# Kernel optimization log

Hardware: AMD Instinct MI355X
Metric: run time of the kernel (lower is better)

The kernel has to match this reference:

```python
import jax, jax.numpy as jnp
import numpy as np

B, N, F_IN = 4, 8000, 3          # batch, electrons per event, (x,y,z) features
HID, S, T = 128, 1024, 1024      # MLP hidden, n_sensors, waveform_ticks
INV_SQRT_2PI = 0.3989422804


def _mlp(x, W1, b1, W2, b2):
    h = jax.nn.relu(x @ W1 + b1)
    return h @ W2 + b2


def setup_inputs() -> dict:
    key = jax.random.key(0)
    ks = jax.random.split(key, 12)
    simulator_input = jax.random.normal(ks[0], (B, N, F_IN), dtype=jnp.float32)
    # z positions in tick units, spread across the waveform
    z_positions = jax.random.uniform(ks[1], (B, N), dtype=jnp.float32) * (T - 1)
    mask = jnp.ones((B, N, 1), dtype=jnp.float32)
    s1 = 1.0 / np.sqrt(F_IN)
    s2 = 1.0 / np.sqrt(HID)
    Wp1 = jax.random.normal(ks[2], (F_IN, HID), dtype=jnp.float32) * s1
    bp1 = jnp.zeros((HID,), dtype=jnp.float32)
    Wp2 = jax.random.normal(ks[3], (HID, S), dtype=jnp.float32) * s2
    bp2 = jnp.zeros((S,), dtype=jnp.float32)
    Wa1 = jax.random.normal(ks[4], (F_IN, HID), dtype=jnp.float32) * s1
    ba1 = jnp.zeros((HID,), dtype=jnp.float32)
    Wa2 = jax.random.normal(ks[5], (HID, S), dtype=jnp.float32) * s2
    ba2 = jnp.zeros((S,), dtype=jnp.float32)
    nn_bin_sigma = 5.0 * jnp.ones((1,), dtype=jnp.float32)  # self.variable init
    return dict(simulator_input=simulator_input, z_positions=z_positions, mask=mask,
                Wp1=Wp1, bp1=bp1, Wp2=Wp2, bp2=bp2,
                Wa1=Wa1, ba1=ba1, Wa2=Wa2, ba2=ba2,
                nn_bin_sigma=nn_bin_sigma)


def reference(simulator_input, z_positions, mask,
              Wp1, bp1, Wp2, bp2, Wa1, ba1, Wa2, ba2, nn_bin_sigma):
    # sensor response per electron: sigmoid(prob MLP) * amp MLP * mask  -> [B,N,S]
    sensor_probs = jax.nn.sigmoid(_mlp(simulator_input, Wp1, bp1, Wp2, bp2))
    el_light_amp = _mlp(simulator_input, Wa1, ba1, Wa2, ba2)
    response_of_sensors = el_light_amp * sensor_probs * mask

    # Gaussian binning kernel over waveform ticks: [B,N,T]
    ticks = jnp.arange(T, dtype=simulator_input.dtype)          # linspace(0, T-1, T)
    sigma = nn_bin_sigma[0]
    diff = ticks[None, None, :] - z_positions[:, :, None]
    exp_values = jnp.exp(-(diff ** 2) / (2.0 * sigma ** 2)) * (INV_SQRT_2PI / jnp.sqrt(sigma ** 2))

    # per-batch waveforms = sensor_response.T @ exp_values -> [B,S,T]; then sum over batch
    waveforms = jnp.einsum('bns,bnt->st', response_of_sensors, exp_values)
    return waveforms  # [S, T]
```

## Files before the change

### kernel.cpp

```cpp
#include <hip/hip_runtime.h>


#define BN_E   32000
#define NBLK   125
#define HIDW   128
#define S_DIM  1024
#define T_DIM  1024
#define NBKT   16
#define KSPL   4
#define MAXPAD (BN_E + NBKT * 31)
#define MAXCG  ((MAXPAD + 31) / 32)
#define INV_SQRT_2PI 0.3989422804f

typedef __attribute__((ext_vector_type(8))) unsigned short u16x8;
typedef __attribute__((ext_vector_type(8))) __bf16         bf16x8;
typedef __attribute__((ext_vector_type(4))) float          f32x4;

static __device__ __forceinline__ unsigned short f2bf(float f) {
    union { float f; unsigned int u; } v; v.f = f;
    unsigned int r = v.u + 0x7FFFu + ((v.u >> 16) & 1u);
    return (unsigned short)(r >> 16);
}

static __device__ __forceinline__ f32x4 mfma16(u16x8 a, u16x8 b, f32x4 c) {
    return __builtin_amdgcn_mfma_f32_16x16x32_bf16(
        __builtin_bit_cast(bf16x8, a), __builtin_bit_cast(bf16x8, b), c, 0, 0, 0);
}

static __device__ __forceinline__ int bucket_of(float z) {
    int b = (int)floorf((z - 31.f) * (1.f / 64.f));
    return min(max(b, 0), NBKT - 1);
}

__global__ __launch_bounds__(256) void k_count(const float* __restrict__ z,
                                               int* __restrict__ bc) {
    int bx = blockIdx.x;
    __shared__ int h[NBKT];
    if (threadIdx.x < NBKT) h[threadIdx.x] = 0;
    __syncthreads();
    int e = bx * 256 + threadIdx.x;
    atomicAdd(&h[bucket_of(z[e])], 1);
    __syncthreads();
    if (threadIdx.x < NBKT) bc[bx * NBKT + threadIdx.x] = h[threadIdx.x];
}

__global__ __launch_bounds__(256) void k_fillscan(const float* __restrict__ z,
                                                  const int* __restrict__ bc,
                                                  int* __restrict__ meta,
                                                  int* __restrict__ list) {
    __shared__ int part[16][16];
    __shared__ int segoff[16][16];
    __shared__ int cntL[NBKT], pstartL[NBKT], baseL[NBKT], h[NBKT];
    int t = threadIdx.x, b = t & 15, seg = t >> 4;
    int v[8]; int sum = 0;
#pragma unroll
    for (int i = 0; i < 8; ++i) {
        int blk = seg * 8 + i;
        v[i] = (blk < NBLK) ? bc[blk * NBKT + b] : 0;
        sum += v[i];
    }
    part[seg][b] = sum;
    if (t < NBKT) h[t] = 0;
    __syncthreads();
    if (t < NBKT) {
        int run = 0;
        for (int s = 0; s < 16; ++s) { segoff[s][t] = run; run += part[s][t]; }
        cntL[t] = run;
    }
    __syncthreads();
    if (t == 0) {
        int s = 0;
        for (int i = 0; i < NBKT; ++i) {
            pstartL[i] = s;
            s += ((cntL[i] + 31) >> 5) << 5;
        }
        if (blockIdx.x == 0) {
            for (int i = 0; i < NBKT; ++i) { meta[i] = cntL[i]; meta[32 + i] = pstartL[i]; }
            meta[48] = s;
        }
    }
    __syncthreads();
    if (t < NBKT) {
        int me = blockIdx.x;
        int run = segoff[me >> 3][t];
        for (int k = 0; k < (me & 7); ++k)
            run += bc[((me >> 3) * 8 + k) * NBKT + t];
        baseL[t] = pstartL[t] + run;
    }
    __syncthreads();
    int e = blockIdx.x * 256 + t;
    int b2 = bucket_of(z[e]);
    int r = atomicAdd(&h[b2], 1);
    list[baseL[b2] + r] = e;
}

__global__ __launch_bounds__(256) void k_prep(
    const float* __restrict__ x, const float* __restrict__ zg,
    const float* __restrict__ maskg, const float* __restrict__ sigp,
    const float* __restrict__ Wp1, const float* __restrict__ bp1,
    const float* __restrict__ Wa1, const float* __restrict__ ba1,
    const float* __restrict__ Wp2, const float* __restrict__ Wa2,
    const int* __restrict__ meta, const int* __restrict__ list,
    unsigned short* __restrict__ HpS, unsigned short* __restrict__ HaS,
    unsigned short* __restrict__ GT,
    unsigned short* __restrict__ WfP, unsigned short* __restrict__ WfA) {
    int bx = blockIdx.x;
    if (bx < MAXCG) {
        int tid = threadIdx.x;

        __shared__ float W1L[1024];
        __shared__ float zzL[32], cmL[32];
        __shared__ int metaL[33];
        if (tid < 33) metaL[tid] = meta[tid < 16 ? tid : (tid < 32 ? tid + 16 : 48)];
        if (tid < 96)                        ((float4*)W1L)[tid]              = ((const float4*)Wp1)[tid];
        else if (tid < 128)                  ((float4*)(W1L + 384))[tid - 96] = ((const float4*)bp1)[tid - 96];
        else if (tid < 224)                  ((float4*)(W1L + 512))[tid - 128]= ((const float4*)Wa1)[tid - 128];
        else                                 ((float4*)(W1L + 896))[tid - 224]= ((const float4*)ba1)[tid - 224];
        __syncthreads();

        int pos0 = bx * 32;
        if (pos0 >= metaL[32]) return;
        int b = 15;
        while (metaL[16 + b] > pos0) --b;
        int tb = b * 64, cnt = metaL[b], pstart = metaL[16 + b];

        if (tid < 32) {
            int pos = pos0 + tid;
            bool real = (pos - pstart) < cnt;
            int ev = real ? list[pos] : 0;
            float sigma = sigp[0];
            zzL[tid] = real ? zg[ev] : 0.f;
            cmL[tid] = real ? (INV_SQRT_2PI / sigma) * maskg[ev] : 0.f;
        }

        {
            int e_l = tid & 31, part = tid >> 5;
            int pos = pos0 + e_l;
            bool real = (pos - pstart) < cnt;
            int ev = real ? list[pos] : 0;
            float x0 = 0.f, x1 = 0.f, x2 = 0.f;
            if (real) { x0 = x[ev * 3]; x1 = x[ev * 3 + 1]; x2 = x[ev * 3 + 2]; }
            unsigned short hp[16], ha[16];
#pragma unroll
            for (int i = 0; i < 16; ++i) {
                int j = part * 16 + i;
                float hv = x0 * W1L[j] + x1 * W1L[128 + j] + x2 * W1L[256 + j] + W1L[384 + j];
                float av = x0 * W1L[512 + j] + x1 * W1L[640 + j] + x2 * W1L[768 + j] + W1L[896 + j];
                hp[i] = real ? f2bf(fmaxf(hv, 0.f)) : (unsigned short)0;
                ha[i] = real ? f2bf(fmaxf(av, 0.f)) : (unsigned short)0;
            }
#pragma unroll
            for (int h2 = 0; h2 < 2; ++h2) {
                int u = (2 * part + h2) * 32 + e_l;
                *(uint4*)&HpS[(size_t)bx * 4096 + u * 8] = ((uint4*)hp)[h2];
                *(uint4*)&HaS[(size_t)bx * 4096 + u * 8] = ((uint4*)ha)[h2];
            }
        }
        __syncthreads();

        {
            float sigma = sigp[0];
            float nis2 = -1.f / (2.f * sigma * sigma);
#pragma unroll
            for (int uu = 0; uu < 2; ++uu) {
                int u = tid * 2 + uu;
                int n8 = u >> 6, q = (u >> 4) & 3, c = u & 15;
                float tt = (float)(tb + n8 * 16 + c);
                unsigned short g8[8];
#pragma unroll
                for (int j = 0; j < 8; ++j) {
                    int e = q * 8 + j;
                    float d = tt - zzL[e];
                    g8[j] = f2bf(cmL[e] * __expf(d * d * nis2));
                }
                *(uint4*)&GT[(size_t)bx * 4096 + u * 8] = *(uint4*)g8;
            }
        }
    } else {
        int bid = bx - MAXCG;
        const float* src = (bid & 64) ? Wa2 : Wp2;
        unsigned short* dst = (bid & 64) ? WfA : WfP;
        int rem = bid & 63;
        int kq = rem >> 2;
        int s  = (rem & 3) * 256 + threadIdx.x;
        int ks = kq >> 2, q = kq & 3;
        unsigned short fr[8];
#pragma unroll
        for (int j = 0; j < 8; ++j)
            fr[j] = f2bf(src[(ks * 32 + q * 8 + j) * S_DIM + s]);
        ((u16x8*)dst)[kq * S_DIM + s] = *(u16x8*)fr;
    }
}

__global__ __launch_bounds__(512, 4) void k_main(
    const unsigned short* __restrict__ HpS, const unsigned short* __restrict__ HaS,
    const unsigned short* __restrict__ WfP, const unsigned short* __restrict__ WfA,
    const float* __restrict__ bp2, const float* __restrict__ ba2,
    const int* __restrict__ meta, const unsigned short* __restrict__ GT,
    float* __restrict__ P) {

    const int bk     = blockIdx.x / KSPL;
    const int kspl   = blockIdx.x % KSPL;
    const int s0     = blockIdx.y * 128;
    const int cnt    = meta[bk];
    const int pstart = meta[32 + bk];
    const int nch    = (cnt + 31) >> 5;
    const int per    = (nch + KSPL - 1) / KSPL;
    const int c0     = kspl * per;
    const int c1     = min(nch, c0 + per);

    const int tid = threadIdx.x;
    const int w = tid >> 6, l = tid & 63, q = l >> 4, c = l & 15;
    const f32x4 z4 = { 0.f, 0.f, 0.f, 0.f };
    float* Pp = P + (size_t)(blockIdx.x * 8 + blockIdx.y) * 16384;

    if (c0 >= c1) {
        f32x4* p4 = (f32x4*)Pp;
#pragma unroll
        for (int i = 0; i < 8; ++i) p4[i * 512 + tid] = z4;
        return;
    }

    __shared__ __align__(16) uint4 HpL[1024];
    __shared__ __align__(16) uint4 HaL[1024];
    __shared__ __align__(16) unsigned short RspL[128 * 40];

    const u16x8* WfPv = (const u16x8*)WfP;
    const u16x8* WfAv = (const u16x8*)WfA;
    const int sg = s0 + w * 16 + c;
    u16x8 wP[4], wA[4];
#pragma unroll
    for (int ks = 0; ks < 4; ++ks) {
        wP[ks] = WfPv[(ks * 4 + q) * S_DIM + sg];
        wA[ks] = WfAv[(ks * 4 + q) * S_DIM + sg];
    }
    const float bp2v = bp2[sg];
    const float ba2v = ba2[sg];

    f32x4 acc2[8];
#pragma unroll
    for (int n8 = 0; n8 < 8; ++n8) acc2[n8] = z4;

    const uint4* Hp4 = (const uint4*)HpS;
    const uint4* Ha4 = (const uint4*)HaS;
    const int cgBase = pstart >> 5;

    size_t cb = (size_t)(cgBase + c0) * 512;
    uint4 p = Hp4[cb + tid];
    uint4 a = Ha4[cb + tid];

    for (int ci = c0; ci < c1; ++ci) {
        const int buf = ((ci - c0) & 1) << 9;
        HpL[buf + tid] = p;
        HaL[buf + tid] = a;

        int nc = min(ci + 1, c1 - 1);
        cb = (size_t)(cgBase + nc) * 512;
        p = Hp4[cb + tid];
        a = Ha4[cb + tid];
        __syncthreads();

        const unsigned short* gt = GT + (size_t)(cgBase + ci) * 4096;
        u16x8 bfr[8];
#pragma unroll
        for (int n8 = 0; n8 < 8; ++n8)
            bfr[n8] = *(const u16x8*)&gt[((n8 * 4 + q) * 16 + c) * 8];

        const u16x8* StHp = (const u16x8*)(HpL + buf);
        const u16x8* StHa = (const u16x8*)(HaL + buf);
        f32x4 aP[2], aA[2];
        aP[0] = z4; aP[1] = z4; aA[0] = z4; aA[1] = z4;
#pragma unroll
        for (int ks = 0; ks < 4; ++ks) {
            u16x8 hp0 = StHp[(ks * 4 + q) * 32 + c];
            u16x8 hp1 = StHp[(ks * 4 + q) * 32 + c + 16];
            u16x8 ha0 = StHa[(ks * 4 + q) * 32 + c];
            u16x8 ha1 = StHa[(ks * 4 + q) * 32 + c + 16];
            aP[0] = mfma16(hp0, wP[ks], aP[0]);
            aP[1] = mfma16(hp1, wP[ks], aP[1]);
            aA[0] = mfma16(ha0, wA[ks], aA[0]);
            aA[1] = mfma16(ha1, wA[ks], aA[1]);
        }

#pragma unroll
        for (int m = 0; m < 2; ++m) {
            f32x4 pp = aP[m], aa = aA[m];
            unsigned long long pk = 0;
#pragma unroll
            for (int r = 0; r < 4; ++r) {
                float pr = pp[r] + bp2v;
                float ar = aa[r] + ba2v;
                float sg2 = __builtin_amdgcn_rcpf(1.f + __expf(-pr));
                pk |= (unsigned long long)f2bf(sg2 * ar) << (16 * r);
            }
            *(unsigned long long*)&RspL[(w * 16 + c) * 40 + m * 16 + q * 4] = pk;
        }

        u16x8 afr = *(const u16x8*)&RspL[(w * 16 + c) * 40 + q * 8];
#pragma unroll
        for (int n8 = 0; n8 < 8; ++n8)
            acc2[n8] = mfma16(afr, bfr[n8], acc2[n8]);
    }

#pragma unroll
    for (int n8 = 0; n8 < 8; ++n8) {
        int tl = n8 * 16 + c;
        int sl = w * 16 + q * 4;
#pragma unroll
        for (int r = 0; r < 4; ++r)
            Pp[(sl + r) * 128 + tl] = acc2[n8][r];
    }
}

__global__ __launch_bounds__(256) void k_reduce(const float* __restrict__ P,
                                                float* __restrict__ out) {
    int idx = blockIdx.x * 256 + threadIdx.x;
    int t0  = (idx & 255) << 2;
    int s   = idx >> 8;
    int bkA = t0 >> 6;
    int colA = t0 & 63;
    int y    = s >> 7;
    int sl   = s & 127;
    const f32x4* P4 = (const f32x4*)P;
    f32x4 acc = { 0.f, 0.f, 0.f, 0.f };
#pragma unroll
    for (int k = 0; k < KSPL; ++k) {
        f32x4 v = P4[((size_t)(bkA * KSPL + k) * 8 + y) * 4096 + sl * 32 + (colA >> 2)];
        acc[0] += v[0]; acc[1] += v[1]; acc[2] += v[2]; acc[3] += v[3];
    }
    if (bkA > 0) {
        int colB = 64 + colA;
#pragma unroll
        for (int k = 0; k < KSPL; ++k) {
            f32x4 v = P4[((size_t)((bkA - 1) * KSPL + k) * 8 + y) * 4096 + sl * 32 + (colB >> 2)];
            acc[0] += v[0]; acc[1] += v[1]; acc[2] += v[2]; acc[3] += v[3];
        }
    }
    ((f32x4*)out)[idx] = acc;
}


extern "C" void kernel_launch(void* const* d_in, const int* in_sizes, int n_in,
                              void* d_out, int out_size, void* d_ws, size_t ws_size,
                              hipStream_t stream) {
    const float* x    = (const float*)d_in[0];
    const float* zp   = (const float*)d_in[1];
    const float* mask = (const float*)d_in[2];
    const float* Wp1  = (const float*)d_in[3];
    const float* bp1  = (const float*)d_in[4];
    const float* Wp2  = (const float*)d_in[5];
    const float* bp2  = (const float*)d_in[6];
    const float* Wa1  = (const float*)d_in[7];
    const float* ba1  = (const float*)d_in[8];
    const float* Wa2  = (const float*)d_in[9];
    const float* ba2  = (const float*)d_in[10];
    const float* sig  = (const float*)d_in[11];

    char* ws = (char*)d_ws;
    unsigned short* HpS  = (unsigned short*)(ws);
    unsigned short* HaS  = (unsigned short*)(ws + 8323072);
    unsigned short* WfP  = (unsigned short*)(ws + 16646144);
    unsigned short* WfA  = (unsigned short*)(ws + 16908288);
    int*            meta = (int*)(ws + 17170432);
    int*            list = (int*)(ws + 17170688);
    int*            bc   = (int*)(ws + 17300736);
    unsigned short* GT   = (unsigned short*)(ws + 17308736);
    float*          P    = (float*)(ws + 25631808);

    k_count<<<NBLK, 256, 0, stream>>>(zp, bc);
    k_fillscan<<<NBLK, 256, 0, stream>>>(zp, bc, meta, list);
    k_prep<<<MAXCG + 128, 256, 0, stream>>>(x, zp, mask, sig,
                                            Wp1, bp1, Wa1, ba1, Wp2, Wa2,
                                            meta, list, HpS, HaS, GT, WfP, WfA);
    k_main<<<dim3(NBKT * KSPL, 8, 1), 512, 0, stream>>>(
        HpS, HaS, WfP, WfA, bp2, ba2, meta, GT, P);
    k_reduce<<<1024, 256, 0, stream>>>(P, (float*)d_out);
}
```

Measured before the change: 145.0 us.

## Merge counting and scatter into one single-block sort, process two chunks per sync

```diff
diff --git a/kernel.cpp b/kernel.cpp
--- a/kernel.cpp
+++ b/kernel.cpp
@@ -2,7 +2,6 @@
 
 
 #define BN_E   32000
-#define NBLK   125
 #define HIDW   128
 #define S_DIM  1024
 #define T_DIM  1024
@@ -32,66 +31,72 @@
     return min(max(b, 0), NBKT - 1);
 }
 
-__global__ __launch_bounds__(256) void k_count(const float* __restrict__ z,
-                                               int* __restrict__ bc) {
-    int bx = blockIdx.x;
-    __shared__ int h[NBKT];
-    if (threadIdx.x < NBKT) h[threadIdx.x] = 0;
-    __syncthreads();
-    int e = bx * 256 + threadIdx.x;
-    atomicAdd(&h[bucket_of(z[e])], 1);
-    __syncthreads();
-    if (threadIdx.x < NBKT) bc[bx * NBKT + threadIdx.x] = h[threadIdx.x];
-}
-
-__global__ __launch_bounds__(256) void k_fillscan(const float* __restrict__ z,
-                                                  const int* __restrict__ bc,
-                                                  int* __restrict__ meta,
-                                                  int* __restrict__ list) {
-    __shared__ int part[16][16];
-    __shared__ int segoff[16][16];
-    __shared__ int cntL[NBKT], pstartL[NBKT], baseL[NBKT], h[NBKT];
-    int t = threadIdx.x, b = t & 15, seg = t >> 4;
-    int v[8]; int sum = 0;
-#pragma unroll
-    for (int i = 0; i < 8; ++i) {
-        int blk = seg * 8 + i;
-        v[i] = (blk < NBLK) ? bc[blk * NBKT + b] : 0;
-        sum += v[i];
-    }
-    part[seg][b] = sum;
-    if (t < NBKT) h[t] = 0;
-    __syncthreads();
-    if (t < NBKT) {
-        int run = 0;
-        for (int s = 0; s < 16; ++s) { segoff[s][t] = run; run += part[s][t]; }
-        cntL[t] = run;
-    }
-    __syncthreads();
-    if (t == 0) {
+__global__ __launch_bounds__(1024) void k_sort(
+    const float* __restrict__ z,
+    const float* __restrict__ Wp2, const float* __restrict__ Wa2,
+    int* __restrict__ meta, int* __restrict__ list,
+    unsigned short* __restrict__ WfP, unsigned short* __restrict__ WfA) {
+    int bx = blockIdx.x, tid = threadIdx.x;
+    if (bx > 0) {
+        int id = (bx - 1) * 1024 + tid;
+        const float* src = (id & 16384) ? Wa2 : Wp2;
+        unsigned short* dst = (id & 16384) ? WfA : WfP;
+        int kq = (id >> 10) & 15;
+        int s  = tid;
+        int ks = kq >> 2, q = kq & 3;
+        unsigned short fr[8];
+#pragma unroll
+        for (int j = 0; j < 8; ++j)
+            fr[j] = f2bf(src[(ks * 32 + q * 8 + j) * S_DIM + s]);
+        ((u16x8*)dst)[kq * S_DIM + s] = *(u16x8*)fr;
+        return;
+    }
+    __shared__ int hist[16][16];
+    __shared__ int cntL[NBKT], pstartL[NBKT];
+    int w = tid >> 6;
+    if (tid < 256) ((int*)hist)[tid] = 0;
+    __syncthreads();
+    if (tid < 1000) {
+#pragma unroll 4
+        for (int i = 0; i < 32; ++i) {
+            int e = i * 1000 + tid;
+            atomicAdd(&hist[w][bucket_of(z[e])], 1);
+        }
+    }
+    __syncthreads();
+    if (tid < NBKT) {
+        int s = 0;
+#pragma unroll
+        for (int w2 = 0; w2 < 16; ++w2) s += hist[w2][tid];
+        cntL[tid] = s;
+    }
+    __syncthreads();
+    if (tid == 0) {
         int s = 0;
         for (int i = 0; i < NBKT; ++i) {
             pstartL[i] = s;
             s += ((cntL[i] + 31) >> 5) << 5;
         }
-        if (blockIdx.x == 0) {
-            for (int i = 0; i < NBKT; ++i) { meta[i] = cntL[i]; meta[32 + i] = pstartL[i]; }
-            meta[48] = s;
-        }
-    }
-    __syncthreads();
-    if (t < NBKT) {
-        int me = blockIdx.x;
-        int run = segoff[me >> 3][t];
-        for (int k = 0; k < (me & 7); ++k)
-            run += bc[((me >> 3) * 8 + k) * NBKT + t];
-        baseL[t] = pstartL[t] + run;
-    }
-    __syncthreads();
-    int e = blockIdx.x * 256 + t;
-    int b2 = bucket_of(z[e]);
-    int r = atomicAdd(&h[b2], 1);
-    list[baseL[b2] + r] = e;
+        meta[48] = s;
+    }
+    __syncthreads();
+    if (tid < NBKT) {
+        meta[tid] = cntL[tid];
+        meta[32 + tid] = pstartL[tid];
+        int run = pstartL[tid];
+#pragma unroll
+        for (int w2 = 0; w2 < 16; ++w2) { int h = hist[w2][tid]; hist[w2][tid] = run; run += h; }
+    }
+    __syncthreads();
+    if (tid < 1000) {
+#pragma unroll 4
+        for (int i = 0; i < 32; ++i) {
+            int e = i * 1000 + tid;
+            int b = bucket_of(z[e]);
+            int r = atomicAdd(&hist[w][b], 1);
+            list[r] = e;
+        }
+    }
 }
 
 __global__ __launch_bounds__(256) void k_prep(
@@ -99,96 +104,79 @@
     const float* __restrict__ maskg, const float* __restrict__ sigp,
     const float* __restrict__ Wp1, const float* __restrict__ bp1,
     const float* __restrict__ Wa1, const float* __restrict__ ba1,
-    const float* __restrict__ Wp2, const float* __restrict__ Wa2,
     const int* __restrict__ meta, const int* __restrict__ list,
     unsigned short* __restrict__ HpS, unsigned short* __restrict__ HaS,
-    unsigned short* __restrict__ GT,
-    unsigned short* __restrict__ WfP, unsigned short* __restrict__ WfA) {
+    unsigned short* __restrict__ GT) {
     int bx = blockIdx.x;
-    if (bx < MAXCG) {
-        int tid = threadIdx.x;
-
-        __shared__ float W1L[1024];
-        __shared__ float zzL[32], cmL[32];
-        __shared__ int metaL[33];
-        if (tid < 33) metaL[tid] = meta[tid < 16 ? tid : (tid < 32 ? tid + 16 : 48)];
-        if (tid < 96)                        ((float4*)W1L)[tid]              = ((const float4*)Wp1)[tid];
-        else if (tid < 128)                  ((float4*)(W1L + 384))[tid - 96] = ((const float4*)bp1)[tid - 96];
-        else if (tid < 224)                  ((float4*)(W1L + 512))[tid - 128]= ((const float4*)Wa1)[tid - 128];
-        else                                 ((float4*)(W1L + 896))[tid - 224]= ((const float4*)ba1)[tid - 224];
-        __syncthreads();
-
-        int pos0 = bx * 32;
-        if (pos0 >= metaL[32]) return;
-        int b = 15;
-        while (metaL[16 + b] > pos0) --b;
-        int tb = b * 64, cnt = metaL[b], pstart = metaL[16 + b];
-
-        if (tid < 32) {
-            int pos = pos0 + tid;
-            bool real = (pos - pstart) < cnt;
-            int ev = real ? list[pos] : 0;
-            float sigma = sigp[0];
-            zzL[tid] = real ? zg[ev] : 0.f;
-            cmL[tid] = real ? (INV_SQRT_2PI / sigma) * maskg[ev] : 0.f;
-        }
-
-        {
-            int e_l = tid & 31, part = tid >> 5;
-            int pos = pos0 + e_l;
-            bool real = (pos - pstart) < cnt;
-            int ev = real ? list[pos] : 0;
-            float x0 = 0.f, x1 = 0.f, x2 = 0.f;
-            if (real) { x0 = x[ev * 3]; x1 = x[ev * 3 + 1]; x2 = x[ev * 3 + 2]; }
-            unsigned short hp[16], ha[16];
-#pragma unroll
-            for (int i = 0; i < 16; ++i) {
-                int j = part * 16 + i;
-                float hv = x0 * W1L[j] + x1 * W1L[128 + j] + x2 * W1L[256 + j] + W1L[384 + j];
-                float av = x0 * W1L[512 + j] + x1 * W1L[640 + j] + x2 * W1L[768 + j] + W1L[896 + j];
-                hp[i] = real ? f2bf(fmaxf(hv, 0.f)) : (unsigned short)0;
-                ha[i] = real ? f2bf(fmaxf(av, 0.f)) : (unsigned short)0;
+    int tid = threadIdx.x;
+
+    __shared__ float W1L[1024];
+    __shared__ float zzL[32], cmL[32];
+    __shared__ int metaL[33];
+    if (tid < 33) metaL[tid] = meta[tid < 16 ? tid : (tid < 32 ? tid + 16 : 48)];
+    if (tid < 96)                        ((float4*)W1L)[tid]              = ((const float4*)Wp1)[tid];
+    else if (tid < 128)                  ((float4*)(W1L + 384))[tid - 96] = ((const float4*)bp1)[tid - 96];
+    else if (tid < 224)                  ((float4*)(W1L + 512))[tid - 128]= ((const float4*)Wa1)[tid - 128];
+    else                                 ((float4*)(W1L + 896))[tid - 224]= ((const float4*)ba1)[tid - 224];
+    __syncthreads();
+
+    int pos0 = bx * 32;
+    if (pos0 >= metaL[32]) return;
+    int b = 15;
+    while (metaL[16 + b] > pos0) --b;
+    int tb = b * 64, cnt = metaL[b], pstart = metaL[16 + b];
+
+    if (tid < 32) {
+        int pos = pos0 + tid;
+        bool real = (pos - pstart) < cnt;
+        int ev = real ? list[pos] : 0;
+        float sigma = sigp[0];
+        zzL[tid] = real ? zg[ev] : 0.f;
+        cmL[tid] = real ? (INV_SQRT_2PI / sigma) * maskg[ev] : 0.f;
+    }
+
+    {
+        int e_l = tid & 31, part = tid >> 5;
+        int pos = pos0 + e_l;
+        bool real = (pos - pstart) < cnt;
+        int ev = real ? list[pos] : 0;
+        float x0 = 0.f, x1 = 0.f, x2 = 0.f;
+        if (real) { x0 = x[ev * 3]; x1 = x[ev * 3 + 1]; x2 = x[ev * 3 + 2]; }
+        unsigned short hp[16], ha[16];
+#pragma unroll
+        for (int i = 0; i < 16; ++i) {
+            int j = part * 16 + i;
+            float hv = x0 * W1L[j] + x1 * W1L[128 + j] + x2 * W1L[256 + j] + W1L[384 + j];
+            float av = x0 * W1L[512 + j] + x1 * W1L[640 + j] + x2 * W1L[768 + j] + W1L[896 + j];
+            hp[i] = real ? f2bf(fmaxf(hv, 0.f)) : (unsigned short)0;
+            ha[i] = real ? f2bf(fmaxf(av, 0.f)) : (unsigned short)0;
+        }
+#pragma unroll
+        for (int h2 = 0; h2 < 2; ++h2) {
+            int u = (2 * part + h2) * 32 + e_l;
+            *(uint4*)&HpS[(size_t)bx * 4096 + u * 8] = ((uint4*)hp)[h2];
+            *(uint4*)&HaS[(size_t)bx * 4096 + u * 8] = ((uint4*)ha)[h2];
+        }
+    }
+    __syncthreads();
+
+    {
+        float sigma = sigp[0];
+        float nis2 = -1.f / (2.f * sigma * sigma);
+#pragma unroll
+        for (int uu = 0; uu < 2; ++uu) {
+            int u = tid * 2 + uu;
+            int n8 = u >> 6, q = (u >> 4) & 3, c = u & 15;
+            float tt = (float)(tb + n8 * 16 + c);
+            unsigned short g8[8];
+#pragma unroll
+            for (int j = 0; j < 8; ++j) {
+                int e = q * 8 + j;
+                float d = tt - zzL[e];
+                g8[j] = f2bf(cmL[e] * __expf(d * d * nis2));
             }
-#pragma unroll
-            for (int h2 = 0; h2 < 2; ++h2) {
-                int u = (2 * part + h2) * 32 + e_l;
-                *(uint4*)&HpS[(size_t)bx * 4096 + u * 8] = ((uint4*)hp)[h2];
-                *(uint4*)&HaS[(size_t)bx * 4096 + u * 8] = ((uint4*)ha)[h2];
-            }
-        }
-        __syncthreads();
-
-        {
-            float sigma = sigp[0];
-            float nis2 = -1.f / (2.f * sigma * sigma);
-#pragma unroll
-            for (int uu = 0; uu < 2; ++uu) {
-                int u = tid * 2 + uu;
-                int n8 = u >> 6, q = (u >> 4) & 3, c = u & 15;
-                float tt = (float)(tb + n8 * 16 + c);
-                unsigned short g8[8];
-#pragma unroll
-                for (int j = 0; j < 8; ++j) {
-                    int e = q * 8 + j;
-                    float d = tt - zzL[e];
-                    g8[j] = f2bf(cmL[e] * __expf(d * d * nis2));
-                }
-                *(uint4*)&GT[(size_t)bx * 4096 + u * 8] = *(uint4*)g8;
-            }
-        }
-    } else {
-        int bid = bx - MAXCG;
-        const float* src = (bid & 64) ? Wa2 : Wp2;
-        unsigned short* dst = (bid & 64) ? WfA : WfP;
-        int rem = bid & 63;
-        int kq = rem >> 2;
-        int s  = (rem & 3) * 256 + threadIdx.x;
-        int ks = kq >> 2, q = kq & 3;
-        unsigned short fr[8];
-#pragma unroll
-        for (int j = 0; j < 8; ++j)
-            fr[j] = f2bf(src[(ks * 32 + q * 8 + j) * S_DIM + s]);
-        ((u16x8*)dst)[kq * S_DIM + s] = *(u16x8*)fr;
+            *(uint4*)&GT[(size_t)bx * 4096 + u * 8] = *(uint4*)g8;
+        }
     }
 }
 
@@ -199,9 +187,11 @@
     const int* __restrict__ meta, const unsigned short* __restrict__ GT,
     float* __restrict__ P) {
 
-    const int bk     = blockIdx.x / KSPL;
-    const int kspl   = blockIdx.x % KSPL;
-    const int s0     = blockIdx.y * 128;
+    const int id     = blockIdx.x;
+    const int bk     = id & 15;
+    const int kspl   = (id >> 4) & 3;
+    const int y      = id >> 6;
+    const int s0     = y * 128;
     const int cnt    = meta[bk];
     const int pstart = meta[32 + bk];
     const int nch    = (cnt + 31) >> 5;
@@ -212,7 +202,7 @@
     const int tid = threadIdx.x;
     const int w = tid >> 6, l = tid & 63, q = l >> 4, c = l & 15;
     const f32x4 z4 = { 0.f, 0.f, 0.f, 0.f };
-    float* Pp = P + (size_t)(blockIdx.x * 8 + blockIdx.y) * 16384;
+    float* Pp = P + (size_t)((bk * KSPL + kspl) * 8 + y) * 16384;
 
     if (c0 >= c1) {
         f32x4* p4 = (f32x4*)Pp;
@@ -221,8 +211,8 @@
         return;
     }
 
-    __shared__ __align__(16) uint4 HpL[1024];
-    __shared__ __align__(16) uint4 HaL[1024];
+    __shared__ __align__(16) uint4 HpL[2048];
+    __shared__ __align__(16) uint4 HaL[2048];
     __shared__ __align__(16) unsigned short RspL[128 * 40];
 
     const u16x8* WfPv = (const u16x8*)WfP;
@@ -245,29 +235,15 @@
     const uint4* Ha4 = (const uint4*)HaS;
     const int cgBase = pstart >> 5;
 
-    size_t cb = (size_t)(cgBase + c0) * 512;
-    uint4 p = Hp4[cb + tid];
-    uint4 a = Ha4[cb + tid];
-
-    for (int ci = c0; ci < c1; ++ci) {
-        const int buf = ((ci - c0) & 1) << 9;
-        HpL[buf + tid] = p;
-        HaL[buf + tid] = a;
-
-        int nc = min(ci + 1, c1 - 1);
-        cb = (size_t)(cgBase + nc) * 512;
-        p = Hp4[cb + tid];
-        a = Ha4[cb + tid];
-        __syncthreads();
-
+    auto do_chunk = [&](int ci, const uint4* hpB, const uint4* haB) {
         const unsigned short* gt = GT + (size_t)(cgBase + ci) * 4096;
         u16x8 bfr[8];
 #pragma unroll
         for (int n8 = 0; n8 < 8; ++n8)
             bfr[n8] = *(const u16x8*)&gt[((n8 * 4 + q) * 16 + c) * 8];
 
-        const u16x8* StHp = (const u16x8*)(HpL + buf);
-        const u16x8* StHa = (const u16x8*)(HaL + buf);
+        const u16x8* StHp = (const u16x8*)hpB;
+        const u16x8* StHa = (const u16x8*)haB;
         f32x4 aP[2], aA[2];
         aP[0] = z4; aP[1] = z4; aA[0] = z4; aA[1] = z4;
 #pragma unroll
@@ -300,6 +276,30 @@
 #pragma unroll
         for (int n8 = 0; n8 < 8; ++n8)
             acc2[n8] = mfma16(afr, bfr[n8], acc2[n8]);
+    };
+
+    {
+        size_t cbA = (size_t)(cgBase + c0) * 512;
+        size_t cbB = (size_t)(cgBase + min(c0 + 1, c1 - 1)) * 512;
+        uint4 pA = Hp4[cbA + tid], aA_ = Ha4[cbA + tid];
+        uint4 pB = Hp4[cbB + tid], aB_ = Ha4[cbB + tid];
+
+        for (int ci = c0; ci < c1; ci += 2) {
+            const int buf = (((ci - c0) >> 1) & 1) << 10;
+            HpL[buf + tid] = pA; HpL[buf + 512 + tid] = pB;
+            HaL[buf + tid] = aA_; HaL[buf + 512 + tid] = aB_;
+
+            int n0 = min(ci + 2, c1 - 1), n1 = min(ci + 3, c1 - 1);
+            size_t nbA = (size_t)(cgBase + n0) * 512;
+            size_t nbB = (size_t)(cgBase + n1) * 512;
+            pA = Hp4[nbA + tid]; aA_ = Ha4[nbA + tid];
+            pB = Hp4[nbB + tid]; aB_ = Ha4[nbB + tid];
+            __syncthreads();
+
+            do_chunk(ci, HpL + buf, HaL + buf);
+            if (ci + 1 < c1)
+                do_chunk(ci + 1, HpL + buf + 512, HaL + buf + 512);
+        }
     }
 
 #pragma unroll
@@ -363,16 +363,14 @@
     unsigned short* WfA  = (unsigned short*)(ws + 16908288);
     int*            meta = (int*)(ws + 17170432);
     int*            list = (int*)(ws + 17170688);
-    int*            bc   = (int*)(ws + 17300736);
     unsigned short* GT   = (unsigned short*)(ws + 17308736);
     float*          P    = (float*)(ws + 25631808);
 
-    k_count<<<NBLK, 256, 0, stream>>>(zp, bc);
-    k_fillscan<<<NBLK, 256, 0, stream>>>(zp, bc, meta, list);
-    k_prep<<<MAXCG + 128, 256, 0, stream>>>(x, zp, mask, sig,
-                                            Wp1, bp1, Wa1, ba1, Wp2, Wa2,
-                                            meta, list, HpS, HaS, GT, WfP, WfA);
-    k_main<<<dim3(NBKT * KSPL, 8, 1), 512, 0, stream>>>(
+    k_sort<<<33, 1024, 0, stream>>>(zp, Wp2, Wa2, meta, list, WfP, WfA);
+    k_prep<<<MAXCG, 256, 0, stream>>>(x, zp, mask, sig,
+                                      Wp1, bp1, Wa1, ba1,
+                                      meta, list, HpS, HaS, GT);
+    k_main<<<512, 512, 0, stream>>>(
         HpS, HaS, WfP, WfA, bp2, ba2, meta, GT, P);
     k_reduce<<<1024, 256, 0, stream>>>(P, (float*)d_out);
 }
```

After: 226.6 us. +56.3%, slower.

## Fuse all five kernels into one cooperative persistent kernel with grid syncs

Applied to the files above, without the earlier changes.

```diff
diff --git a/kernel.cpp b/kernel.cpp
--- a/kernel.cpp
+++ b/kernel.cpp
@@ -1,9 +1,11 @@
 #include <hip/hip_runtime.h>
+#include <hip/hip_cooperative_groups.h>
+
+namespace cg = cooperative_groups;
 
 
 #define BN_E   32000
 #define NBLK   125
-#define HIDW   128
 #define S_DIM  1024
 #define T_DIM  1024
 #define NBKT   16
@@ -32,157 +34,37 @@
     return min(max(b, 0), NBKT - 1);
 }
 
-__global__ __launch_bounds__(256) void k_count(const float* __restrict__ z,
-                                               int* __restrict__ bc) {
-    int bx = blockIdx.x;
-    __shared__ int h[NBKT];
-    if (threadIdx.x < NBKT) h[threadIdx.x] = 0;
-    __syncthreads();
-    int e = bx * 256 + threadIdx.x;
-    atomicAdd(&h[bucket_of(z[e])], 1);
-    __syncthreads();
-    if (threadIdx.x < NBKT) bc[bx * NBKT + threadIdx.x] = h[threadIdx.x];
-}
-
-__global__ __launch_bounds__(256) void k_fillscan(const float* __restrict__ z,
-                                                  const int* __restrict__ bc,
-                                                  int* __restrict__ meta,
-                                                  int* __restrict__ list) {
-    __shared__ int part[16][16];
-    __shared__ int segoff[16][16];
-    __shared__ int cntL[NBKT], pstartL[NBKT], baseL[NBKT], h[NBKT];
-    int t = threadIdx.x, b = t & 15, seg = t >> 4;
-    int v[8]; int sum = 0;
-#pragma unroll
-    for (int i = 0; i < 8; ++i) {
-        int blk = seg * 8 + i;
-        v[i] = (blk < NBLK) ? bc[blk * NBKT + b] : 0;
-        sum += v[i];
-    }
-    part[seg][b] = sum;
-    if (t < NBKT) h[t] = 0;
-    __syncthreads();
-    if (t < NBKT) {
-        int run = 0;
-        for (int s = 0; s < 16; ++s) { segoff[s][t] = run; run += part[s][t]; }
-        cntL[t] = run;
-    }
-    __syncthreads();
-    if (t == 0) {
-        int s = 0;
-        for (int i = 0; i < NBKT; ++i) {
-            pstartL[i] = s;
-            s += ((cntL[i] + 31) >> 5) << 5;
-        }
-        if (blockIdx.x == 0) {
-            for (int i = 0; i < NBKT; ++i) { meta[i] = cntL[i]; meta[32 + i] = pstartL[i]; }
-            meta[48] = s;
-        }
-    }
-    __syncthreads();
-    if (t < NBKT) {
-        int me = blockIdx.x;
-        int run = segoff[me >> 3][t];
-        for (int k = 0; k < (me & 7); ++k)
-            run += bc[((me >> 3) * 8 + k) * NBKT + t];
-        baseL[t] = pstartL[t] + run;
-    }
-    __syncthreads();
-    int e = blockIdx.x * 256 + t;
-    int b2 = bucket_of(z[e]);
-    int r = atomicAdd(&h[b2], 1);
-    list[baseL[b2] + r] = e;
-}
-
-__global__ __launch_bounds__(256) void k_prep(
-    const float* __restrict__ x, const float* __restrict__ zg,
+__global__ __launch_bounds__(512, 2) void k_all(
+    const float* __restrict__ x, const float* __restrict__ zp,
     const float* __restrict__ maskg, const float* __restrict__ sigp,
     const float* __restrict__ Wp1, const float* __restrict__ bp1,
     const float* __restrict__ Wa1, const float* __restrict__ ba1,
     const float* __restrict__ Wp2, const float* __restrict__ Wa2,
-    const int* __restrict__ meta, const int* __restrict__ list,
+    const float* __restrict__ bp2, const float* __restrict__ ba2,
+    int* __restrict__ meta, int* __restrict__ list, int* __restrict__ bc,
     unsigned short* __restrict__ HpS, unsigned short* __restrict__ HaS,
     unsigned short* __restrict__ GT,
-    unsigned short* __restrict__ WfP, unsigned short* __restrict__ WfA) {
-    int bx = blockIdx.x;
-    if (bx < MAXCG) {
-        int tid = threadIdx.x;
-
-        __shared__ float W1L[1024];
-        __shared__ float zzL[32], cmL[32];
-        __shared__ int metaL[33];
-        if (tid < 33) metaL[tid] = meta[tid < 16 ? tid : (tid < 32 ? tid + 16 : 48)];
-        if (tid < 96)                        ((float4*)W1L)[tid]              = ((const float4*)Wp1)[tid];
-        else if (tid < 128)                  ((float4*)(W1L + 384))[tid - 96] = ((const float4*)bp1)[tid - 96];
-        else if (tid < 224)                  ((float4*)(W1L + 512))[tid - 128]= ((const float4*)Wa1)[tid - 128];
-        else                                 ((float4*)(W1L + 896))[tid - 224]= ((const float4*)ba1)[tid - 224];
-        __syncthreads();
-
-        int pos0 = bx * 32;
-        if (pos0 >= metaL[32]) return;
-        int b = 15;
-        while (metaL[16 + b] > pos0) --b;
-        int tb = b * 64, cnt = metaL[b], pstart = metaL[16 + b];
-
-        if (tid < 32) {
-            int pos = pos0 + tid;
-            bool real = (pos - pstart) < cnt;
-            int ev = real ? list[pos] : 0;
-            float sigma = sigp[0];
-            zzL[tid] = real ? zg[ev] : 0.f;
-            cmL[tid] = real ? (INV_SQRT_2PI / sigma) * maskg[ev] : 0.f;
-        }
-
-        {
-            int e_l = tid & 31, part = tid >> 5;
-            int pos = pos0 + e_l;
-            bool real = (pos - pstart) < cnt;
-            int ev = real ? list[pos] : 0;
-            float x0 = 0.f, x1 = 0.f, x2 = 0.f;
-            if (real) { x0 = x[ev * 3]; x1 = x[ev * 3 + 1]; x2 = x[ev * 3 + 2]; }
-            unsigned short hp[16], ha[16];
-#pragma unroll
-            for (int i = 0; i < 16; ++i) {
-                int j = part * 16 + i;
-                float hv = x0 * W1L[j] + x1 * W1L[128 + j] + x2 * W1L[256 + j] + W1L[384 + j];
-                float av = x0 * W1L[512 + j] + x1 * W1L[640 + j] + x2 * W1L[768 + j] + W1L[896 + j];
-                hp[i] = real ? f2bf(fmaxf(hv, 0.f)) : (unsigned short)0;
-                ha[i] = real ? f2bf(fmaxf(av, 0.f)) : (unsigned short)0;
-            }
-#pragma unroll
-            for (int h2 = 0; h2 < 2; ++h2) {
-                int u = (2 * part + h2) * 32 + e_l;
-                *(uint4*)&HpS[(size_t)bx * 4096 + u * 8] = ((uint4*)hp)[h2];
-                *(uint4*)&HaS[(size_t)bx * 4096 + u * 8] = ((uint4*)ha)[h2];
-            }
-        }
-        __syncthreads();
-
-        {
-            float sigma = sigp[0];
-            float nis2 = -1.f / (2.f * sigma * sigma);
-#pragma unroll
-            for (int uu = 0; uu < 2; ++uu) {
-                int u = tid * 2 + uu;
-                int n8 = u >> 6, q = (u >> 4) & 3, c = u & 15;
-                float tt = (float)(tb + n8 * 16 + c);
-                unsigned short g8[8];
-#pragma unroll
-                for (int j = 0; j < 8; ++j) {
-                    int e = q * 8 + j;
-                    float d = tt - zzL[e];
-                    g8[j] = f2bf(cmL[e] * __expf(d * d * nis2));
-                }
-                *(uint4*)&GT[(size_t)bx * 4096 + u * 8] = *(uint4*)g8;
-            }
-        }
-    } else {
-        int bid = bx - MAXCG;
-        const float* src = (bid & 64) ? Wa2 : Wp2;
-        unsigned short* dst = (bid & 64) ? WfA : WfP;
-        int rem = bid & 63;
-        int kq = rem >> 2;
-        int s  = (rem & 3) * 256 + threadIdx.x;
+    unsigned short* __restrict__ WfP, unsigned short* __restrict__ WfA,
+    float* __restrict__ P, float* __restrict__ out)
+{
+    __shared__ __align__(16) unsigned char SMEM[43008];
+    const int bx = blockIdx.x, tid = threadIdx.x;
+    cg::grid_group grid = cg::this_grid();
+    const f32x4 z4 = { 0.f, 0.f, 0.f, 0.f };
+
+    if (bx < NBLK) {
+        int* hist = (int*)SMEM;
+        if (tid < NBKT) hist[tid] = 0;
+        __syncthreads();
+        if (tid < 256) atomicAdd(&hist[bucket_of(zp[bx * 256 + tid])], 1);
+        __syncthreads();
+        if (tid < NBKT) bc[bx * NBKT + tid] = hist[tid];
+    } else if (bx >= 192) {
+        int id = (bx - 192) * 512 + tid;
+        const float* src = (id >> 14) ? Wa2 : Wp2;
+        unsigned short* dst = (id >> 14) ? WfA : WfP;
+        int kq = (id >> 10) & 15;
+        int s  = id & 1023;
         int ks = kq >> 2, q = kq & 3;
         unsigned short fr[8];
 #pragma unroll
@@ -190,153 +72,290 @@
             fr[j] = f2bf(src[(ks * 32 + q * 8 + j) * S_DIM + s]);
         ((u16x8*)dst)[kq * S_DIM + s] = *(u16x8*)fr;
     }
-}
-
-__global__ __launch_bounds__(512, 4) void k_main(
-    const unsigned short* __restrict__ HpS, const unsigned short* __restrict__ HaS,
-    const unsigned short* __restrict__ WfP, const unsigned short* __restrict__ WfA,
-    const float* __restrict__ bp2, const float* __restrict__ ba2,
-    const int* __restrict__ meta, const unsigned short* __restrict__ GT,
-    float* __restrict__ P) {
-
-    const int bk     = blockIdx.x / KSPL;
-    const int kspl   = blockIdx.x % KSPL;
-    const int s0     = blockIdx.y * 128;
-    const int cnt    = meta[bk];
-    const int pstart = meta[32 + bk];
-    const int nch    = (cnt + 31) >> 5;
-    const int per    = (nch + KSPL - 1) / KSPL;
-    const int c0     = kspl * per;
-    const int c1     = min(nch, c0 + per);
-
-    const int tid = threadIdx.x;
-    const int w = tid >> 6, l = tid & 63, q = l >> 4, c = l & 15;
-    const f32x4 z4 = { 0.f, 0.f, 0.f, 0.f };
-    float* Pp = P + (size_t)(blockIdx.x * 8 + blockIdx.y) * 16384;
-
-    if (c0 >= c1) {
-        f32x4* p4 = (f32x4*)Pp;
-#pragma unroll
-        for (int i = 0; i < 8; ++i) p4[i * 512 + tid] = z4;
-        return;
-    }
-
-    __shared__ __align__(16) uint4 HpL[1024];
-    __shared__ __align__(16) uint4 HaL[1024];
-    __shared__ __align__(16) unsigned short RspL[128 * 40];
-
-    const u16x8* WfPv = (const u16x8*)WfP;
-    const u16x8* WfAv = (const u16x8*)WfA;
-    const int sg = s0 + w * 16 + c;
-    u16x8 wP[4], wA[4];
-#pragma unroll
-    for (int ks = 0; ks < 4; ++ks) {
-        wP[ks] = WfPv[(ks * 4 + q) * S_DIM + sg];
-        wA[ks] = WfAv[(ks * 4 + q) * S_DIM + sg];
-    }
-    const float bp2v = bp2[sg];
-    const float ba2v = ba2[sg];
-
-    f32x4 acc2[8];
-#pragma unroll
-    for (int n8 = 0; n8 < 8; ++n8) acc2[n8] = z4;
-
-    const uint4* Hp4 = (const uint4*)HpS;
-    const uint4* Ha4 = (const uint4*)HaS;
-    const int cgBase = pstart >> 5;
-
-    size_t cb = (size_t)(cgBase + c0) * 512;
-    uint4 p = Hp4[cb + tid];
-    uint4 a = Ha4[cb + tid];
-
-    for (int ci = c0; ci < c1; ++ci) {
-        const int buf = ((ci - c0) & 1) << 9;
-        HpL[buf + tid] = p;
-        HaL[buf + tid] = a;
-
-        int nc = min(ci + 1, c1 - 1);
-        cb = (size_t)(cgBase + nc) * 512;
-        p = Hp4[cb + tid];
-        a = Ha4[cb + tid];
-        __syncthreads();
-
-        const unsigned short* gt = GT + (size_t)(cgBase + ci) * 4096;
-        u16x8 bfr[8];
-#pragma unroll
-        for (int n8 = 0; n8 < 8; ++n8)
-            bfr[n8] = *(const u16x8*)&gt[((n8 * 4 + q) * 16 + c) * 8];
-
-        const u16x8* StHp = (const u16x8*)(HpL + buf);
-        const u16x8* StHa = (const u16x8*)(HaL + buf);
-        f32x4 aP[2], aA[2];
-        aP[0] = z4; aP[1] = z4; aA[0] = z4; aA[1] = z4;
-#pragma unroll
-        for (int ks = 0; ks < 4; ++ks) {
-            u16x8 hp0 = StHp[(ks * 4 + q) * 32 + c];
-            u16x8 hp1 = StHp[(ks * 4 + q) * 32 + c + 16];
-            u16x8 ha0 = StHa[(ks * 4 + q) * 32 + c];
-            u16x8 ha1 = StHa[(ks * 4 + q) * 32 + c + 16];
-            aP[0] = mfma16(hp0, wP[ks], aP[0]);
-            aP[1] = mfma16(hp1, wP[ks], aP[1]);
-            aA[0] = mfma16(ha0, wA[ks], aA[0]);
-            aA[1] = mfma16(ha1, wA[ks], aA[1]);
-        }
-
-#pragma unroll
-        for (int m = 0; m < 2; ++m) {
-            f32x4 pp = aP[m], aa = aA[m];
-            unsigned long long pk = 0;
-#pragma unroll
-            for (int r = 0; r < 4; ++r) {
-                float pr = pp[r] + bp2v;
-                float ar = aa[r] + ba2v;
-                float sg2 = __builtin_amdgcn_rcpf(1.f + __expf(-pr));
-                pk |= (unsigned long long)f2bf(sg2 * ar) << (16 * r);
-            }
-            *(unsigned long long*)&RspL[(w * 16 + c) * 40 + m * 16 + q * 4] = pk;
-        }
-
-        u16x8 afr = *(const u16x8*)&RspL[(w * 16 + c) * 40 + q * 8];
-#pragma unroll
-        for (int n8 = 0; n8 < 8; ++n8)
-            acc2[n8] = mfma16(afr, bfr[n8], acc2[n8]);
-    }
-
-#pragma unroll
-    for (int n8 = 0; n8 < 8; ++n8) {
-        int tl = n8 * 16 + c;
-        int sl = w * 16 + q * 4;
-#pragma unroll
-        for (int r = 0; r < 4; ++r)
-            Pp[(sl + r) * 128 + tl] = acc2[n8][r];
-    }
-}
-
-__global__ __launch_bounds__(256) void k_reduce(const float* __restrict__ P,
-                                                float* __restrict__ out) {
-    int idx = blockIdx.x * 256 + threadIdx.x;
-    int t0  = (idx & 255) << 2;
-    int s   = idx >> 8;
-    int bkA = t0 >> 6;
-    int colA = t0 & 63;
-    int y    = s >> 7;
-    int sl   = s & 127;
-    const f32x4* P4 = (const f32x4*)P;
-    f32x4 acc = { 0.f, 0.f, 0.f, 0.f };
-#pragma unroll
-    for (int k = 0; k < KSPL; ++k) {
-        f32x4 v = P4[((size_t)(bkA * KSPL + k) * 8 + y) * 4096 + sl * 32 + (colA >> 2)];
-        acc[0] += v[0]; acc[1] += v[1]; acc[2] += v[2]; acc[3] += v[3];
-    }
-    if (bkA > 0) {
-        int colB = 64 + colA;
-#pragma unroll
-        for (int k = 0; k < KSPL; ++k) {
-            f32x4 v = P4[((size_t)((bkA - 1) * KSPL + k) * 8 + y) * 4096 + sl * 32 + (colB >> 2)];
-            acc[0] += v[0]; acc[1] += v[1]; acc[2] += v[2]; acc[3] += v[3];
-        }
-    }
-    ((f32x4*)out)[idx] = acc;
+    grid.sync();
+
+    if (bx < NBLK) {
+        int* part    = (int*)SMEM;
+        int* segoff  = part + 256;
+        int* cntL    = segoff + 256;
+        int* pstartL = cntL + 16;
+        int* baseL   = pstartL + 16;
+        int* h       = baseL + 16;
+        int t = tid, b = t & 15, seg = (t >> 4) & 15;
+        if (t < 256) {
+            int sum = 0;
+#pragma unroll
+            for (int i = 0; i < 8; ++i) {
+                int blk = seg * 8 + i;
+                sum += (blk < NBLK) ? bc[blk * NBKT + b] : 0;
+            }
+            part[seg * 16 + b] = sum;
+            if (t < NBKT) h[t] = 0;
+        }
+        __syncthreads();
+        if (t < NBKT) {
+            int run = 0;
+            for (int s = 0; s < 16; ++s) { segoff[s * 16 + t] = run; run += part[s * 16 + t]; }
+            cntL[t] = run;
+        }
+        __syncthreads();
+        if (t == 0) {
+            int s = 0;
+            for (int i = 0; i < NBKT; ++i) {
+                pstartL[i] = s;
+                s += ((cntL[i] + 31) >> 5) << 5;
+            }
+            if (bx == 0) meta[48] = s;
+        }
+        __syncthreads();
+        if (t < NBKT) {
+            if (bx == 0) { meta[t] = cntL[t]; meta[32 + t] = pstartL[t]; }
+            int me = bx;
+            int run = segoff[(me >> 3) * 16 + t];
+            for (int k = 0; k < (me & 7); ++k)
+                run += bc[((me >> 3) * 8 + k) * NBKT + t];
+            baseL[t] = pstartL[t] + run;
+        }
+        __syncthreads();
+        if (t < 256) {
+            int e = bx * 256 + t;
+            int b2 = bucket_of(zp[e]);
+            int r = atomicAdd(&h[b2], 1);
+            list[baseL[b2] + r] = e;
+        }
+    }
+    grid.sync();
+
+    {
+        float* W1L   = (float*)SMEM;
+        int*   metaL = (int*)(SMEM + 4096);
+        float* zzA   = (float*)(SMEM + 4352);
+        float* cmA   = (float*)(SMEM + 4608);
+        if (tid < 33) metaL[tid] = meta[tid < 16 ? tid : (tid < 32 ? tid + 16 : 48)];
+        if (tid < 96)       ((float4*)W1L)[tid]               = ((const float4*)Wp1)[tid];
+        else if (tid < 128) ((float4*)(W1L + 384))[tid - 96]  = ((const float4*)bp1)[tid - 96];
+        else if (tid < 224) ((float4*)(W1L + 512))[tid - 128] = ((const float4*)Wa1)[tid - 128];
+        else if (tid < 256) ((float4*)(W1L + 896))[tid - 224] = ((const float4*)ba1)[tid - 224];
+        __syncthreads();
+
+        int lane = tid >> 8, lt = tid & 255;
+        float* zzL = zzA + lane * 32;
+        float* cmL = cmA + lane * 32;
+        int total = metaL[32];
+        float sigma = sigp[0];
+        float nis2 = -1.f / (2.f * sigma * sigma);
+
+        for (int j = 0; j < 2; ++j) {
+            int ck = bx * 4 + lane * 2 + j;
+            int pos0 = ck * 32;
+            bool act = (ck < MAXCG) && (pos0 < total);
+            int tb = 0, cnt = 0, pstart = 0;
+            if (act) {
+                int b = 15;
+                while (metaL[16 + b] > pos0) --b;
+                tb = b * 64; cnt = metaL[b]; pstart = metaL[16 + b];
+            }
+            __syncthreads();
+            if (act && lt < 32) {
+                int pos = pos0 + lt;
+                bool real = (pos - pstart) < cnt;
+                int ev = real ? list[pos] : 0;
+                zzL[lt] = real ? zp[ev] : 0.f;
+                cmL[lt] = real ? (INV_SQRT_2PI / sigma) * maskg[ev] : 0.f;
+            }
+            if (act) {
+                int e_l = lt & 31, part = lt >> 5;
+                int pos = pos0 + e_l;
+                bool real = (pos - pstart) < cnt;
+                int ev = real ? list[pos] : 0;
+                float x0 = 0.f, x1 = 0.f, x2 = 0.f;
+                if (real) { x0 = x[ev * 3]; x1 = x[ev * 3 + 1]; x2 = x[ev * 3 + 2]; }
+                unsigned short hp[16], ha[16];
+#pragma unroll
+                for (int i = 0; i < 16; ++i) {
+                    int jj = part * 16 + i;
+                    float hv = x0 * W1L[jj] + x1 * W1L[128 + jj] + x2 * W1L[256 + jj] + W1L[384 + jj];
+                    float av = x0 * W1L[512 + jj] + x1 * W1L[640 + jj] + x2 * W1L[768 + jj] + W1L[896 + jj];
+                    hp[i] = real ? f2bf(fmaxf(hv, 0.f)) : (unsigned short)0;
+                    ha[i] = real ? f2bf(fmaxf(av, 0.f)) : (unsigned short)0;
+                }
+#pragma unroll
+                for (int h2 = 0; h2 < 2; ++h2) {
+                    int u = (2 * part + h2) * 32 + e_l;
+                    *(uint4*)&HpS[(size_t)ck * 4096 + u * 8] = ((uint4*)hp)[h2];
+                    *(uint4*)&HaS[(size_t)ck * 4096 + u * 8] = ((uint4*)ha)[h2];
+                }
+            }
+            __syncthreads();
+            if (act) {
+#pragma unroll
+                for (int uu = 0; uu < 2; ++uu) {
+                    int u = lt * 2 + uu;
+                    int n8 = u >> 6, q = (u >> 4) & 3, c = u & 15;
+                    float tt = (float)(tb + n8 * 16 + c);
+                    unsigned short g8[8];
+#pragma unroll
+                    for (int jj = 0; jj < 8; ++jj) {
+                        int e = q * 8 + jj;
+                        float d = tt - zzL[e];
+                        g8[jj] = f2bf(cmL[e] * __expf(d * d * nis2));
+                    }
+                    *(uint4*)&GT[(size_t)ck * 4096 + u * 8] = *(uint4*)g8;
+                }
+            }
+        }
+    }
+    grid.sync();
+
+    {
+        uint4* HpL = (uint4*)SMEM;
+        uint4* HaL = (uint4*)(SMEM + 16384);
+        unsigned short* RspL = (unsigned short*)(SMEM + 32768);
+
+        const int w = tid >> 6, l = tid & 63, q = l >> 4, c = l & 15;
+        const uint4* Hp4 = (const uint4*)HpS;
+        const uint4* Ha4 = (const uint4*)HaS;
+        const u16x8* WfPv = (const u16x8*)WfP;
+        const u16x8* WfAv = (const u16x8*)WfA;
+
+        auto run_tile = [&](int T) {
+            const int xq   = T & 63;
+            const int bk   = xq >> 2;
+            const int kspl = xq & 3;
+            const int y    = T >> 6;
+            const int s0   = y * 128;
+            const int cnt    = meta[bk];
+            const int pstart = meta[32 + bk];
+            const int nch  = (cnt + 31) >> 5;
+            const int per  = (nch + KSPL - 1) / KSPL;
+            const int c0   = kspl * per;
+            const int c1   = min(nch, c0 + per);
+            float* Pp = P + (size_t)((bk * KSPL + kspl) * 8 + y) * 16384;
+
+            if (c0 >= c1) {
+                f32x4* p4 = (f32x4*)Pp;
+#pragma unroll
+                for (int i = 0; i < 8; ++i) p4[i * 512 + tid] = z4;
+                return;
+            }
+
+            const int sg = s0 + w * 16 + c;
+            u16x8 wP[4], wA[4];
+#pragma unroll
+            for (int ks = 0; ks < 4; ++ks) {
+                wP[ks] = WfPv[(ks * 4 + q) * S_DIM + sg];
+                wA[ks] = WfAv[(ks * 4 + q) * S_DIM + sg];
+            }
+            const float bp2v = bp2[sg];
+            const float ba2v = ba2[sg];
+
+            f32x4 acc2[8];
+#pragma unroll
+            for (int n8 = 0; n8 < 8; ++n8) acc2[n8] = z4;
+
+            const int cgBase = pstart >> 5;
+
+            size_t cb = (size_t)(cgBase + c0) * 512;
+            uint4 p = Hp4[cb + tid];
+            uint4 a = Ha4[cb + tid];
+
+            for (int ci = c0; ci < c1; ++ci) {
+                const int buf = ((ci - c0) & 1) << 9;
+                HpL[buf + tid] = p;
+                HaL[buf + tid] = a;
+
+                int nc = min(ci + 1, c1 - 1);
+                cb = (size_t)(cgBase + nc) * 512;
+                p = Hp4[cb + tid];
+                a = Ha4[cb + tid];
+                __syncthreads();
+
+                const unsigned short* gt = GT + (size_t)(cgBase + ci) * 4096;
+                u16x8 bfr[8];
+#pragma unroll
+                for (int n8 = 0; n8 < 8; ++n8)
+                    bfr[n8] = *(const u16x8*)&gt[((n8 * 4 + q) * 16 + c) * 8];
+
+                const u16x8* StHp = (const u16x8*)(HpL + buf);
+                const u16x8* StHa = (const u16x8*)(HaL + buf);
+                f32x4 aP[2], aA[2];
+                aP[0] = z4; aP[1] = z4; aA[0] = z4; aA[1] = z4;
+#pragma unroll
+                for (int ks = 0; ks < 4; ++ks) {
+                    u16x8 hp0 = StHp[(ks * 4 + q) * 32 + c];
+                    u16x8 hp1 = StHp[(ks * 4 + q) * 32 + c + 16];
+                    u16x8 ha0 = StHa[(ks * 4 + q) * 32 + c];
+                    u16x8 ha1 = StHa[(ks * 4 + q) * 32 + c + 16];
+                    aP[0] = mfma16(hp0, wP[ks], aP[0]);
+                    aP[1] = mfma16(hp1, wP[ks], aP[1]);
+                    aA[0] = mfma16(ha0, wA[ks], aA[0]);
+                    aA[1] = mfma16(ha1, wA[ks], aA[1]);
+                }
+
+#pragma unroll
+                for (int m = 0; m < 2; ++m) {
+                    f32x4 pp = aP[m], aa = aA[m];
+                    unsigned long long pk = 0;
+#pragma unroll
+                    for (int r = 0; r < 4; ++r) {
+                        float pr = pp[r] + bp2v;
+                        float ar = aa[r] + ba2v;
+                        float sg2 = __builtin_amdgcn_rcpf(1.f + __expf(-pr));
+                        pk |= (unsigned long long)f2bf(sg2 * ar) << (16 * r);
+                    }
+                    *(unsigned long long*)&RspL[(w * 16 + c) * 40 + m * 16 + q * 4] = pk;
+                }
+
+                u16x8 afr = *(const u16x8*)&RspL[(w * 16 + c) * 40 + q * 8];
+#pragma unroll
+                for (int n8 = 0; n8 < 8; ++n8)
+                    acc2[n8] = mfma16(afr, bfr[n8], acc2[n8]);
+            }
+
+#pragma unroll
+            for (int n8 = 0; n8 < 8; ++n8) {
+                int tl = n8 * 16 + c;
+                int sl = w * 16 + q * 4;
+#pragma unroll
+                for (int r = 0; r < 4; ++r)
+                    Pp[(sl + r) * 128 + tl] = acc2[n8][r];
+            }
+        };
+
+        run_tile(bx);
+        __syncthreads();
+        run_tile(256 + (bx ^ 32));
+    }
+    grid.sync();
+
+    {
+        const f32x4* P4 = (const f32x4*)P;
+#pragma unroll
+        for (int rr = 0; rr < 2; ++rr) {
+            int idx = bx * 1024 + rr * 512 + tid;
+            int t0  = (idx & 255) << 2;
+            int s   = idx >> 8;
+            int bkA = t0 >> 6;
+            int colA = t0 & 63;
+            int y    = s >> 7;
+            int sl   = s & 127;
+            f32x4 acc = { 0.f, 0.f, 0.f, 0.f };
+#pragma unroll
+            for (int k = 0; k < KSPL; ++k) {
+                f32x4 v = P4[((size_t)(bkA * KSPL + k) * 8 + y) * 4096 + sl * 32 + (colA >> 2)];
+                acc[0] += v[0]; acc[1] += v[1]; acc[2] += v[2]; acc[3] += v[3];
+            }
+            if (bkA > 0) {
+                int colB = 64 + colA;
+#pragma unroll
+                for (int k = 0; k < KSPL; ++k) {
+                    f32x4 v = P4[((size_t)((bkA - 1) * KSPL + k) * 8 + y) * 4096 + sl * 32 + (colB >> 2)];
+                    acc[0] += v[0]; acc[1] += v[1]; acc[2] += v[2]; acc[3] += v[3];
+                }
+            }
+            ((f32x4*)out)[idx] = acc;
+        }
+    }
 }
 
 
@@ -366,13 +385,15 @@
     int*            bc   = (int*)(ws + 17300736);
     unsigned short* GT   = (unsigned short*)(ws + 17308736);
     float*          P    = (float*)(ws + 25631808);
-
-    k_count<<<NBLK, 256, 0, stream>>>(zp, bc);
-    k_fillscan<<<NBLK, 256, 0, stream>>>(zp, bc, meta, list);
-    k_prep<<<MAXCG + 128, 256, 0, stream>>>(x, zp, mask, sig,
-                                            Wp1, bp1, Wa1, ba1, Wp2, Wa2,
-                                            meta, list, HpS, HaS, GT, WfP, WfA);
-    k_main<<<dim3(NBKT * KSPL, 8, 1), 512, 0, stream>>>(
-        HpS, HaS, WfP, WfA, bp2, ba2, meta, GT, P);
-    k_reduce<<<1024, 256, 0, stream>>>(P, (float*)d_out);
-}
+    float*          outp = (float*)d_out;
+
+    void* args[] = {
+        (void*)&x, (void*)&zp, (void*)&mask, (void*)&sig,
+        (void*)&Wp1, (void*)&bp1, (void*)&Wa1, (void*)&ba1,
+        (void*)&Wp2, (void*)&Wa2, (void*)&bp2, (void*)&ba2,
+        (void*)&meta, (void*)&list, (void*)&bc,
+        (void*)&HpS, (void*)&HaS, (void*)&GT, (void*)&WfP, (void*)&WfA,
+        (void*)&P, (void*)&outp
+    };
+    hipLaunchCooperativeKernel((void*)k_all, dim3(256), dim3(512), args, 0, stream);
+}
```

After: 303.5 us. 2.09x slower.
